# Kernel optimization log

Measured on AMD Instinct MI355X. Metric: run time of the kernel, lower is better.

The kernel has to match this reference:

```python
import jax, jax.numpy as jnp
import numpy as np

B = 32768   # batch
F = 32      # per-node feature dim
H = 256     # hidden width
M = 4       # modules per node
OUT = 8     # final output dim
INIT_W = 0.003
B_INIT = 0.1


def _lin(k, din, dout):
    # fanin_init-style uniform weights, bias filled with 0.1 (hidden layers)
    s = 1.0 / np.sqrt(din)
    W = jax.random.uniform(k, (M, din, dout), jnp.float32, -s, s)
    b = jnp.full((M, dout), B_INIT, jnp.float32)
    return W, b


def setup_inputs() -> dict:
    key = jax.random.key(0)
    ks = jax.random.split(key, 16)
    feats = jax.random.normal(ks[0], (B, 4 * F), jnp.float32)
    idx = jax.random.randint(ks[1], (B, 4), 0, M)
    onehots = jax.nn.one_hot(idx, M, dtype=jnp.float32).reshape(B, 4 * M)
    input_val = jnp.concatenate([feats, onehots], axis=1)  # [B,144]

    W00, b00 = _lin(ks[2], F, H)        # node0 post layer 0
    W01, b01 = _lin(ks[3], H, H)        # node0 post layer 1
    Wpre1, bpre1 = _lin(ks[4], F, H)    # node1 pre
    Wpost1, bpost1 = _lin(ks[5], 2 * H, H)  # node1 interface (prev 256 + own 256)
    Wpre2, bpre2 = _lin(ks[6], F, H)
    Wpost2, bpost2 = _lin(ks[7], 2 * H, H)
    Wpre3, bpre3 = _lin(ks[8], F, H)
    Wpost3, bpost3 = _lin(ks[9], 2 * H, H)
    # final output layer: uniform(-init_w, init_w) for W and b, identity act
    Wfin3 = jax.random.uniform(ks[10], (M, H, OUT), jnp.float32, -INIT_W, INIT_W)
    bfin3 = jax.random.uniform(ks[11], (M, OUT), jnp.float32, -INIT_W, INIT_W)
    return dict(input_val=input_val,
                W00=W00, b00=b00, W01=W01, b01=b01,
                Wpre1=Wpre1, bpre1=bpre1, Wpost1=Wpost1, bpost1=bpost1,
                Wpre2=Wpre2, bpre2=bpre2, Wpost2=Wpost2, bpost2=bpost2,
                Wpre3=Wpre3, bpre3=bpre3, Wpost3=Wpost3, bpost3=bpost3,
                Wfin3=Wfin3, bfin3=bfin3)


def _select(h, onehot):
    # per-row pick of the assigned module's output: [B,M,D],[B,M] -> [B,D]
    return jnp.einsum('bmo,bm->bo', h, onehot)


def reference(input_val, W00, b00, W01, b01,
              Wpre1, bpre1, Wpost1, bpost1,
              Wpre2, bpre2, Wpost2, bpost2,
              Wpre3, bpre3, Wpost3, bpost3,
              Wfin3, bfin3):
    feat = lambda j: input_val[:, j * F:(j + 1) * F]
    oh = lambda j: input_val[:, 4 * F + j * M: 4 * F + (j + 1) * M]

    # node 0: two hidden layers, module-dispatched (dense-all-modules + one-hot combine)
    h = jax.nn.relu(jnp.einsum('bi,mio->bmo', feat(0), W00) + b00)
    h = jax.nn.relu(jnp.einsum('bmi,mio->bmo', h, W01) + b01)
    x = _select(h, oh(0))  # [B,H]

    def node(x_prev, fj, ohj, Wpre, bpre, Wpost, bpost):
        hp = jax.nn.relu(jnp.einsum('bi,mio->bmo', fj, Wpre) + bpre)
        # interface layer consumes concat([x_prev, hp]); split the weight to
        # avoid materializing [B,M,2H]
        hq = jax.nn.relu(jnp.einsum('bi,mio->bmo', x_prev, Wpost[:, :H, :])
                         + jnp.einsum('bmi,mio->bmo', hp, Wpost[:, H:, :])
                         + bpost)
        return hq  # [B,M,H]

    x = _select(node(x, feat(1), oh(1), Wpre1, bpre1, Wpost1, bpost1), oh(1))
    x = _select(node(x, feat(2), oh(2), Wpre2, bpre2, Wpost2, bpost2), oh(2))

    h3 = node(x, feat(3), oh(3), Wpre3, bpre3, Wpost3, bpost3)  # [B,M,H]
    out = jnp.einsum('bmi,mio->bmo', h3, Wfin3) + bfin3          # final linear, identity act
    return _select(out, oh(3))  # [B,OUT]
```

## Files before the change

### kernel.cpp

```cpp
#include <hip/hip_runtime.h>

#define NB 32768
#define MAXTILE 768
#define ROWS 64
#define NT 4

typedef short s8v __attribute__((ext_vector_type(8)));
typedef short s4v __attribute__((ext_vector_type(4)));
typedef float f4v __attribute__((ext_vector_type(4)));
typedef unsigned short u16;
typedef unsigned short u16x4 __attribute__((ext_vector_type(4)));
typedef unsigned int u32;
typedef unsigned char u8;

__device__ __forceinline__ float bf2f(u16 u) { return __uint_as_float(((u32)u) << 16); }
__device__ __forceinline__ u16 f2bf(float f) {
    u32 x = __float_as_uint(f);
    x += 0x7FFFu + ((x >> 16) & 1u);
    return (u16)(x >> 16);
}
__device__ __forceinline__ s8v ld8(const u16* p) { return *reinterpret_cast<const s8v*>(p); }

#define MFMA16(a, b, c) __builtin_amdgcn_mfma_f32_16x16x32_bf16((a), (b), (c), 0, 0, 0)

template <int N> struct IC { static constexpr int v = N; };

__device__ __forceinline__ void detect_flag(const void* input, int tid, int* shflag)
{
    if (tid < 64) {
        u32 w = ((const u32*)input)[tid];
        u32 h0 = w & 0xFFFFu;
        u32 e0 = (h0 >> 7) & 0xFFu;
        bool plaus = (h0 == 0u) || (e0 >= 96u && e0 <= 143u);
        unsigned long long m = __ballot(plaus);
        if (tid == 0) *shflag = (__popcll(m) >= 48) ? 1 : 0;
    }
}

struct RepArgs {
    const void* W01; const void* Wp[3]; const void* pre[4]; const void* fin;
    const void* bias[9];
    u16 *rPre, *rW01, *rWp[3], *rFin, *cbias;
};

__global__ __launch_bounds__(256) void prepA_kernel(const void* __restrict__ inputv,
                                                    int* __restrict__ gcnt,
                                                    int* __restrict__ perm2,
                                                    u16* __restrict__ feats16,
                                                    RepArgs R)
{
    __shared__ int lcnt[256];
    __shared__ int sBase[256];
    __shared__ u16 T[8192];
    __shared__ int shmisc;
    int tid = threadIdx.x;
    int b = blockIdx.x;
    detect_flag(inputv, tid, &shmisc);
    __syncthreads();
    int flag = shmisc;

    if (b < 128) {
        lcnt[tid] = 0;
        __syncthreads();
        int row = (b << 8) + tid;
        const u32* in32 = (const u32*)inputv;
        const u16* in16 = (const u16*)inputv;
        int key = 0;
        if (flag) {
#pragma unroll
            for (int j = 0; j < 4; j++) {
                u16x4 v = *(const u16x4*)(in16 + row * 144 + 128 + j * 4);
                int m = v[1] ? 1 : (v[2] ? 2 : (v[3] ? 3 : 0));
                key |= m << (j << 1);
            }
        } else {
#pragma unroll
            for (int j = 0; j < 4; j++) {
                const u32* p = in32 + row * 144 + 128 + j * 4;
                u32 v1 = p[1], v2 = p[2], v3 = p[3];
                int m = v1 ? 1 : (v2 ? 2 : (v3 ? 3 : 0));
                key |= m << (j << 1);
            }
        }
        int loc = atomicAdd(&lcnt[key], 1);
        __syncthreads();
        int c = lcnt[tid];
        sBase[tid] = c ? atomicAdd(&gcnt[tid], c) : 0;
        __syncthreads();
        int slot = sBase[key] + loc;
        if (slot < 512) perm2[(key << 9) + slot] = row;

        int r0 = b << 8;
        if (flag) {
            for (int i = tid; i < 256 * 16; i += 256) {
                int r = r0 + (i >> 4), j = (i & 15) << 3;
                *(s8v*)(feats16 + ((size_t)r << 7) + j) = ld8(in16 + (size_t)r * 144 + j);
            }
        } else {
            for (int i = tid; i < 256 * 32; i += 256) {
                int r = r0 + (i >> 5), j = (i & 31) << 2;
                f4v f = *(const f4v*)(in32 + (size_t)r * 144 + j);
                s4v p;
#pragma unroll
                for (int q = 0; q < 4; q++) p[q] = (short)f2bf(f[q]);
                *(s4v*)(feats16 + ((size_t)r << 7) + j) = p;
            }
        }
        return;
    }

    int rb = b - 128;
    const void* src = nullptr; u16* dst = nullptr; int K = 0, k0 = 0, mrow = 0;
    if (rb < 32) {
        int m = rb >> 3, s = rb & 7;
        src = R.W01; dst = R.rW01 + (m * 8 + s) * 8192; K = 256; k0 = s * 32; mrow = m;
    } else if (rb < 224) {
        int idx = rb - 32, mat = idx >> 6, r = idx & 63, m = r >> 4, s = r & 15;
        src = R.Wp[mat]; dst = R.rWp[mat] + (m * 16 + s) * 8192; K = 512; k0 = s * 32; mrow = m;
    } else if (rb < 240) {
        int idx = rb - 224, mat = idx >> 2, m = idx & 3;
        src = R.pre[mat]; dst = R.rPre + (mat * 4 + m) * 8192; K = 32; k0 = 0; mrow = m;
    } else if (rb < 244) {
        int m = rb - 240;
        const u16* s16 = (const u16*)R.fin;
        const float* s32 = (const float*)R.fin;
        for (int i = tid; i < 2048; i += 256) {
            int si = (m * 256 + (i >> 3)) * 8 + (i & 7);
            T[i] = flag ? s16[si] : f2bf(s32[si]);
        }
        __syncthreads();
        u16* d = R.rFin + m * 4096;
        for (int i = tid; i < 4096; i += 256) {
            int s = i >> 9, lane = (i >> 3) & 63, j = i & 7;
            int q = lane >> 4, l16 = lane & 15;
            int k = s * 32 + q * 8 + j;
            d[i] = (l16 < 8) ? T[k * 8 + l16] : (u16)0;
        }
        return;
    } else {
        const int sz[9] = {1024,1024,1024,1024,1024,1024,1024,1024,32};
        const int of[9] = {0,1024,2048,3072,4096,5120,6144,7168,8192};
        for (int i = tid; i < 8224; i += 256) {
            int t = i, e = 0;
            while (t >= sz[e]) { t -= sz[e]; e++; }
            R.cbias[of[e] + t] = flag ? ((const u16*)R.bias[e])[t]
                                      : f2bf(((const float*)R.bias[e])[t]);
        }
        return;
    }
    const u16* s16 = (const u16*)src;
    const float* s32 = (const float*)src;
    for (int i = tid; i < 8192; i += 256) {
        int k = i >> 8, n = i & 255;
        int srcIdx = (mrow * K + k0 + k) * 256 + n;
        T[i] = flag ? s16[srcIdx] : f2bf(s32[srcIdx]);
    }
    __syncthreads();
    for (int i = tid; i < 8192; i += 256) {
        int mt = i >> 9, lane = (i >> 3) & 63, j = i & 7;
        int k = ((lane >> 4) << 3) + j, n = (mt << 4) + (lane & 15);
        dst[i] = T[(k << 8) + n];
    }
}

struct MainP { const u16 *rPre, *rW01, *rWp1, *rWp2, *rWp3, *rFin, *cbias, *feats; };

__global__ __launch_bounds__(512, 4) void main_kernel(
    const void* __restrict__ inRaw,
    const int* __restrict__ gcnt, const int* __restrict__ perm2,
    MainP P, void* __restrict__ outp)
{
    __shared__ __align__(16) u16 xhB[32768];
    __shared__ int rowids[ROWS];
    __shared__ int shflag;
    __shared__ int sMeta[4];

    int tid = threadIdx.x;
    int lane = tid & 63, w = tid >> 6, quad = lane >> 4, l16 = lane & 15;

    int b = blockIdx.x;
    int t = ((b & 7) * (MAXTILE / 8)) + (b >> 3);

    detect_flag(inRaw, tid, &shflag);

    if (tid < 64) {
        int4 g = *(const int4*)(gcnt + tid * 4);
        int tot4[4] = {g.x, g.y, g.z, g.w};
        int tiles4[4], lsum = 0;
#pragma unroll
        for (int j = 0; j < 4; j++) { tiles4[j] = (tot4[j] + 63) >> 6; lsum += tiles4[j]; }
        int pre = lsum;
#pragma unroll
        for (int off = 1; off < 64; off <<= 1) {
            int v = __shfl_up(pre, off, 64);
            if (tid >= off) pre += v;
        }
        int run = pre - lsum;
#pragma unroll
        for (int j = 0; j < 4; j++) {
            if (t >= run && t < run + tiles4[j]) {
                sMeta[0] = tid * 4 + j;
                sMeta[1] = t - run;
                sMeta[2] = tot4[j];
            }
            run += tiles4[j];
        }
        if (tid == 63) sMeta[3] = pre;
    }
    __syncthreads();
    if (t >= sMeta[3]) return;
    int key = sMeta[0], tau = sMeta[1], tot = sMeta[2];
    int cntIn = tot - tau * ROWS; if (cntIn > ROWS) cntIn = ROWS;
    if (tid < ROWS) {
        int g = tid < cntIn ? tid : cntIn - 1;
        rowids[tid] = perm2[(key << 9) + tau * ROWS + g];
    }
    __syncthreads();

    int flag = shflag;
    int rows_[NT];
#pragma unroll
    for (int nt = 0; nt < NT; nt++) rows_[nt] = rowids[nt * 16 + l16];

    const u16* feats = P.feats;
    int mt0 = w << 1, mt1 = mt0 + 1;
    int stA = ((quad >> 1) * 16 + l16) * 8 + (quad & 1) * 4;

    f4v acc0[NT], acc1[NT];

    auto gemm_run = [&](auto nc, const u16* Ab, int ks0) {
        constexpr int N = decltype(nc)::v;
        constexpr int D = 4;
        const u16* base0 = Ab + mt0 * 512 + lane * 8;
        const u16* base1 = Ab + mt1 * 512 + lane * 8;
        s8v A0[D], A1[D];
#pragma unroll
        for (int d = 0; d < D && d < N; d++) {
            A0[d] = ld8(base0 + d * 8192);
            A1[d] = ld8(base1 + d * 8192);
        }
        __syncthreads();
        __builtin_amdgcn_s_setprio(1);
#pragma unroll
        for (int s = 0; s < N; s++) {
            s8v c0 = A0[s % D], c1 = A1[s % D];
            if (s + D < N) {
                A0[s % D] = ld8(base0 + (s + D) * 8192);
                A1[s % D] = ld8(base1 + (s + D) * 8192);
            }
#pragma unroll
            for (int nt = 0; nt < NT; nt++) {
                s8v B = ld8(&xhB[((nt * 16 + ks0 + s) << 9) + lane * 8]);
                acc0[nt] = MFMA16(c0, B, acc0[nt]);
                acc1[nt] = MFMA16(c1, B, acc1[nt]);
            }
        }
        __builtin_amdgcn_s_setprio(0);
    };

    for (int node = 0; node < 4; node++) {
        int m = (key >> (node << 1)) & 3;

        s8v fb[NT];
#pragma unroll
        for (int nt = 0; nt < NT; nt++)
            fb[nt] = ld8(feats + ((size_t)rows_[nt] << 7) + (node << 5) + (quad << 3));

        const u16* preB = P.rPre + ((node << 2) + m) * 8192;
#pragma unroll
        for (int ci = 0; ci < 2; ci++) {
            int mt = mt0 + ci;
            s8v a = ld8(preB + mt * 512 + lane * 8);
            u16x4 bv = *(const u16x4*)(P.cbias + node * 2048 + m * 256 + mt * 16 + quad * 4);
            f4v bias;
#pragma unroll
            for (int r = 0; r < 4; r++) bias[r] = bf2f(bv[r]);
#pragma unroll
            for (int nt = 0; nt < NT; nt++) {
                f4v c = MFMA16(a, fb[nt], bias);
                s4v p;
#pragma unroll
                for (int r = 0; r < 4; r++) { float v = c[r] > 0.f ? c[r] : 0.f; p[r] = (short)f2bf(v); }
                *(s4v*)&xhB[(((nt * 16 + 8 + w) << 9)) + ci * 256 + stA] = p;
            }
        }

        {
            u16x4 b0 = *(const u16x4*)(P.cbias + node * 2048 + 1024 + m * 256 + mt0 * 16 + quad * 4);
            u16x4 b1 = *(const u16x4*)(P.cbias + node * 2048 + 1024 + m * 256 + mt1 * 16 + quad * 4);
            f4v f0, f1;
#pragma unroll
            for (int r = 0; r < 4; r++) { f0[r] = bf2f(b0[r]); f1[r] = bf2f(b1[r]); }
#pragma unroll
            for (int nt = 0; nt < NT; nt++) { acc0[nt] = f0; acc1[nt] = f1; }
        }

        if (node == 0) gemm_run(IC<8>{},  P.rW01 + m * 8 * 8192, 8);
        else {
            const u16* WB = (node == 1 ? P.rWp1 : (node == 2 ? P.rWp2 : P.rWp3)) + m * 16 * 8192;
            gemm_run(IC<16>{}, WB, 0);
        }
        __syncthreads();

#pragma unroll
        for (int ci = 0; ci < 2; ci++) {
#pragma unroll
            for (int nt = 0; nt < NT; nt++) {
                f4v a = ci ? acc1[nt] : acc0[nt];
                s4v p;
#pragma unroll
                for (int r = 0; r < 4; r++) { float v = a[r] > 0.f ? a[r] : 0.f; p[r] = (short)f2bf(v); }
                *(s4v*)&xhB[((nt * 16 + w) << 9) + ci * 256 + stA] = p;
            }
        }
    }
    __syncthreads();

    if (w < NT) {
        int m3 = (key >> 6) & 3;
        f4v c;
#pragma unroll
        for (int r = 0; r < 4; r++)
            c[r] = (quad < 2) ? bf2f(P.cbias[8192 + m3 * 8 + quad * 4 + r]) : 0.f;
#pragma unroll
        for (int s = 0; s < 8; s++) {
            s8v A = ld8(P.rFin + m3 * 4096 + s * 512 + lane * 8);
            s8v B = ld8(&xhB[((w * 16 + s) << 9) + lane * 8]);
            c = MFMA16(A, B, c);
        }
        int bidx = w * 16 + l16;
        if (quad < 2 && bidx < cntIn) {
            int row = rowids[bidx];
            if (flag) {
                s4v p;
#pragma unroll
                for (int r = 0; r < 4; r++) p[r] = (short)f2bf(c[r]);
                *(s4v*)((u16*)outp + row * 8 + quad * 4) = p;
            } else {
                *(f4v*)((float*)outp + row * 8 + quad * 4) = c;
            }
        }
    }
}

extern "C" void kernel_launch(void* const* d_in, const int* in_sizes, int n_in,
                              void* d_out, int out_size, void* d_ws, size_t ws_size,
                              hipStream_t stream)
{
    (void)in_sizes; (void)n_in; (void)out_size;
    const void* input  = d_in[0];
    const void* W00    = d_in[1];
    const void* b00    = d_in[2];
    const void* W01    = d_in[3];
    const void* b01    = d_in[4];
    const void* Wpre1  = d_in[5];
    const void* bpre1  = d_in[6];
    const void* Wpost1 = d_in[7];
    const void* bpost1 = d_in[8];
    const void* Wpre2  = d_in[9];
    const void* bpre2  = d_in[10];
    const void* Wpost2 = d_in[11];
    const void* bpost2 = d_in[12];
    const void* Wpre3  = d_in[13];
    const void* bpre3  = d_in[14];
    const void* Wpost3 = d_in[15];
    const void* bpost3 = d_in[16];
    const void* Wfin   = d_in[17];
    const void* bfin   = d_in[18];

    char* base = (char*)d_ws;
    size_t off = 0;
    auto alloc = [&](size_t bytes) -> char* {
        char* p = base + off;
        off += (bytes + 255) & ~(size_t)255;
        return p;
    };
    int*  gcnt      = (int*)alloc(256 * 4);
    int*  perm2     = (int*)alloc(256 * 512 * 4);
    u16*  feats16   = (u16*)alloc((size_t)NB * 128 * 2);
    u16*  cbias    = (u16*)alloc(8224 * 2);
    u16*  rPre     = (u16*)alloc(131072 * 2);
    u16*  rW01     = (u16*)alloc(262144 * 2);
    u16*  rWp1     = (u16*)alloc(524288 * 2);
    u16*  rWp2     = (u16*)alloc(524288 * 2);
    u16*  rWp3     = (u16*)alloc(524288 * 2);
    u16*  rFin     = (u16*)alloc(16384 * 2);
    if (off > ws_size) return;

    RepArgs R;
    R.W01 = W01; R.Wp[0] = Wpost1; R.Wp[1] = Wpost2; R.Wp[2] = Wpost3;
    R.pre[0] = W00; R.pre[1] = Wpre1; R.pre[2] = Wpre2; R.pre[3] = Wpre3;
    R.fin = Wfin;
    R.bias[0] = b00;   R.bias[1] = b01;
    R.bias[2] = bpre1; R.bias[3] = bpost1;
    R.bias[4] = bpre2; R.bias[5] = bpost2;
    R.bias[6] = bpre3; R.bias[7] = bpost3;
    R.bias[8] = bfin;
    R.rPre = rPre; R.rW01 = rW01;
    R.rWp[0] = rWp1; R.rWp[1] = rWp2; R.rWp[2] = rWp3;
    R.rFin = rFin; R.cbias = cbias;

    hipMemsetAsync(gcnt, 0, 256 * 4, stream);
    prepA_kernel<<<373, 256, 0, stream>>>(input, gcnt, perm2, feats16, R);

    MainP P;
    P.rPre = rPre; P.rW01 = rW01; P.rWp1 = rWp1; P.rWp2 = rWp2; P.rWp3 = rWp3;
    P.rFin = rFin; P.cbias = cbias; P.feats = feats16;
    main_kernel<<<MAXTILE, 512, 0, stream>>>(input, gcnt, perm2, P, d_out);
}
```

Measured before the change: 190.1 us.

## Halve LDS activation buffer by splitting interface GEMM into two sequential halves

The 2H-wide interface GEMM is split into two K=256 passes. The first pass consumes the previous node's activations, then the pre-layer output overwrites the same LDS region and the second pass consumes it. This halves the shared activation buffer from 64KB to 32KB and raises the launch bound to 8 blocks per CU to increase occupancy. In exchange it adds extra block barriers per node, serializes the pre-layer behind the first GEMM half, and shortens the A-operand prefetch depth from 4 to 2.

```diff
diff --git a/kernel.cpp b/kernel.cpp
--- a/kernel.cpp
+++ b/kernel.cpp
@@ -22,8 +22,6 @@
 __device__ __forceinline__ s8v ld8(const u16* p) { return *reinterpret_cast<const s8v*>(p); }
 
 #define MFMA16(a, b, c) __builtin_amdgcn_mfma_f32_16x16x32_bf16((a), (b), (c), 0, 0, 0)
-
-template <int N> struct IC { static constexpr int v = N; };
 
 __device__ __forceinline__ void detect_flag(const void* input, int tid, int* shflag)
 {
@@ -165,12 +163,12 @@
 
 struct MainP { const u16 *rPre, *rW01, *rWp1, *rWp2, *rWp3, *rFin, *cbias, *feats; };
 
-__global__ __launch_bounds__(512, 4) void main_kernel(
+__global__ __launch_bounds__(512, 8) void main_kernel(
     const void* __restrict__ inRaw,
     const int* __restrict__ gcnt, const int* __restrict__ perm2,
     MainP P, void* __restrict__ outp)
 {
-    __shared__ __align__(16) u16 xhB[32768];
+    __shared__ __align__(16) u16 xhB[16384];
     __shared__ int rowids[ROWS];
     __shared__ int shflag;
     __shared__ int sMeta[4];
@@ -228,29 +226,23 @@
 
     f4v acc0[NT], acc1[NT];
 
-    auto gemm_run = [&](auto nc, const u16* Ab, int ks0) {
-        constexpr int N = decltype(nc)::v;
-        constexpr int D = 4;
+    auto gemm_run = [&](const u16* Ab) {
         const u16* base0 = Ab + mt0 * 512 + lane * 8;
         const u16* base1 = Ab + mt1 * 512 + lane * 8;
-        s8v A0[D], A1[D];
-#pragma unroll
-        for (int d = 0; d < D && d < N; d++) {
-            A0[d] = ld8(base0 + d * 8192);
-            A1[d] = ld8(base1 + d * 8192);
-        }
-        __syncthreads();
+        s8v A0[2], A1[2];
+        A0[0] = ld8(base0);        A1[0] = ld8(base1);
+        A0[1] = ld8(base0 + 8192); A1[1] = ld8(base1 + 8192);
         __builtin_amdgcn_s_setprio(1);
 #pragma unroll
-        for (int s = 0; s < N; s++) {
-            s8v c0 = A0[s % D], c1 = A1[s % D];
-            if (s + D < N) {
-                A0[s % D] = ld8(base0 + (s + D) * 8192);
-                A1[s % D] = ld8(base1 + (s + D) * 8192);
+        for (int s = 0; s < 8; s++) {
+            s8v c0 = A0[s & 1], c1 = A1[s & 1];
+            if (s + 2 < 8) {
+                A0[s & 1] = ld8(base0 + (s + 2) * 8192);
+                A1[s & 1] = ld8(base1 + (s + 2) * 8192);
             }
 #pragma unroll
             for (int nt = 0; nt < NT; nt++) {
-                s8v B = ld8(&xhB[((nt * 16 + ks0 + s) << 9) + lane * 8]);
+                s8v B = ld8(&xhB[((nt * 8 + s) << 9) + lane * 8]);
                 acc0[nt] = MFMA16(c0, B, acc0[nt]);
                 acc1[nt] = MFMA16(c1, B, acc1[nt]);
             }
@@ -260,30 +252,6 @@
 
     for (int node = 0; node < 4; node++) {
         int m = (key >> (node << 1)) & 3;
-
-        s8v fb[NT];
-#pragma unroll
-        for (int nt = 0; nt < NT; nt++)
-            fb[nt] = ld8(feats + ((size_t)rows_[nt] << 7) + (node << 5) + (quad << 3));
-
-        const u16* preB = P.rPre + ((node << 2) + m) * 8192;
-#pragma unroll
-        for (int ci = 0; ci < 2; ci++) {
-            int mt = mt0 + ci;
-            s8v a = ld8(preB + mt * 512 + lane * 8);
-            u16x4 bv = *(const u16x4*)(P.cbias + node * 2048 + m * 256 + mt * 16 + quad * 4);
-            f4v bias;
-#pragma unroll
-            for (int r = 0; r < 4; r++) bias[r] = bf2f(bv[r]);
-#pragma unroll
-            for (int nt = 0; nt < NT; nt++) {
-                f4v c = MFMA16(a, fb[nt], bias);
-                s4v p;
-#pragma unroll
-                for (int r = 0; r < 4; r++) { float v = c[r] > 0.f ? c[r] : 0.f; p[r] = (short)f2bf(v); }
-                *(s4v*)&xhB[(((nt * 16 + 8 + w) << 9)) + ci * 256 + stA] = p;
-            }
-        }
 
         {
             u16x4 b0 = *(const u16x4*)(P.cbias + node * 2048 + 1024 + m * 256 + mt0 * 16 + quad * 4);
@@ -295,11 +263,43 @@
             for (int nt = 0; nt < NT; nt++) { acc0[nt] = f0; acc1[nt] = f1; }
         }
 
-        if (node == 0) gemm_run(IC<8>{},  P.rW01 + m * 8 * 8192, 8);
-        else {
+        const u16* wb2;
+        if (node > 0) {
             const u16* WB = (node == 1 ? P.rWp1 : (node == 2 ? P.rWp2 : P.rWp3)) + m * 16 * 8192;
-            gemm_run(IC<16>{}, WB, 0);
-        }
+            gemm_run(WB);
+            __syncthreads();
+            wb2 = WB + 8 * 8192;
+        } else {
+            wb2 = P.rW01 + m * 8 * 8192;
+        }
+
+        {
+            s8v fb[NT];
+#pragma unroll
+            for (int nt = 0; nt < NT; nt++)
+                fb[nt] = ld8(feats + ((size_t)rows_[nt] << 7) + (node << 5) + (quad << 3));
+            const u16* preB = P.rPre + ((node << 2) + m) * 8192;
+#pragma unroll
+            for (int ci = 0; ci < 2; ci++) {
+                int mt = mt0 + ci;
+                s8v a = ld8(preB + mt * 512 + lane * 8);
+                u16x4 bv = *(const u16x4*)(P.cbias + node * 2048 + m * 256 + mt * 16 + quad * 4);
+                f4v bias;
+#pragma unroll
+                for (int r = 0; r < 4; r++) bias[r] = bf2f(bv[r]);
+#pragma unroll
+                for (int nt = 0; nt < NT; nt++) {
+                    f4v c = MFMA16(a, fb[nt], bias);
+                    s4v p;
+#pragma unroll
+                    for (int r = 0; r < 4; r++) { float v = c[r] > 0.f ? c[r] : 0.f; p[r] = (short)f2bf(v); }
+                    *(s4v*)&xhB[((nt * 8 + w) << 9) + ci * 256 + stA] = p;
+                }
+            }
+        }
+        __syncthreads();
+
+        gemm_run(wb2);
         __syncthreads();
 
 #pragma unroll
@@ -310,11 +310,11 @@
                 s4v p;
 #pragma unroll
                 for (int r = 0; r < 4; r++) { float v = a[r] > 0.f ? a[r] : 0.f; p[r] = (short)f2bf(v); }
-                *(s4v*)&xhB[((nt * 16 + w) << 9) + ci * 256 + stA] = p;
-            }
-        }
-    }
-    __syncthreads();
+                *(s4v*)&xhB[((nt * 8 + w) << 9) + ci * 256 + stA] = p;
+            }
+        }
+        __syncthreads();
+    }
 
     if (w < NT) {
         int m3 = (key >> 6) & 3;
@@ -325,7 +325,7 @@
 #pragma unroll
         for (int s = 0; s < 8; s++) {
             s8v A = ld8(P.rFin + m3 * 4096 + s * 512 + lane * 8);
-            s8v B = ld8(&xhB[((w * 16 + s) << 9) + lane * 8]);
+            s8v B = ld8(&xhB[((w * 8 + s) << 9) + lane * 8]);
             c = MFMA16(A, B, c);
         }
         int bidx = w * 16 + l16;
```

Measured after the change: 258.9 us. 36.2% more time.
